# Kernel tuning notes

Measured on AMD Instinct MI355X. Metric: run time of the kernel, lower is better.

## Reference

```python
import jax, jax.numpy as jnp
import numpy as np

B, T, D_IN, D, OUT, L, NDAYS = 32, 2048, 512, 256, 41, 3, 45
INNER = 2 * D  # expand=2

def silu(x):
    return x * jax.nn.sigmoid(x)

def layernorm(x, s, b, eps=1e-5):
    m = x.mean(-1, keepdims=True)
    v = ((x - m) ** 2).mean(-1, keepdims=True)
    return (x - m) / jnp.sqrt(v + eps) * s + b

def dwconv(x, k, b):
    # x: [B,T,C], k: [C,4] depthwise kernel, b: [C]
    # torch Conv1d(padding=2)[..., :T] == pad (left=2, right=1), valid window 4
    y = jax.lax.conv_general_dilated(
        x.transpose(0, 2, 1), k[:, None, :], window_strides=(1,),
        padding=[(2, 1)], feature_group_count=k.shape[0],
        dimension_numbers=('NCH', 'OIH', 'NCH'))
    return y.transpose(0, 2, 1) + b

def soft_window(x, Win, convK, convB, dtW, dtB, Wout):
    # x: [B,T,D]
    xz = x @ Win                      # [B,T,2*INNER]
    xi, z = jnp.split(xz, 2, axis=-1)
    xc = silu(dwconv(xi, convK, convB))
    dt = jax.nn.softplus(xc @ dtW + dtB)
    w = jnp.exp(-jnp.cumsum(dt, axis=1) * 0.1)
    return (xc * w * silu(z)) @ Wout  # [B,T,D]

def setup_inputs() -> dict:
    key = jax.random.key(0)
    ks = iter(jax.random.split(key, 40))
    n = lambda shp, s=0.02: jax.random.normal(next(ks), shp, dtype=jnp.float32) * s
    inp = {}
    inp['x'] = jax.random.normal(next(ks), (B, T, D_IN), dtype=jnp.float32)
    inp['day_ids'] = jax.random.randint(next(ks), (B,), 0, NDAYS)
    inp['adapter_W'] = jnp.tile(jnp.eye(D_IN)[None], (NDAYS, 1, 1)) + n((NDAYS, D_IN, D_IN))
    inp['adapter_b'] = n((NDAYS, D_IN))
    inp['cW1'] = n((D_IN, D)); inp['cb1'] = n((D,))
    inp['cln1_s'] = jnp.ones((D,)); inp['cln1_b'] = jnp.zeros((D,))
    inp['cW2'] = n((D, D)); inp['cb2'] = n((D,))
    inp['cln2_s'] = jnp.ones((D,)); inp['cln2_b'] = jnp.zeros((D,))
    # mamba params: leading dims [L, 2] for (fwd, bwd) directions
    inp['m_in'] = n((L, 2, D, 2 * INNER))
    inp['m_convK'] = n((L, 2, INNER, 4), 0.2); inp['m_convB'] = n((L, 2, INNER))
    inp['m_dtW'] = n((L, 2, INNER, INNER)); inp['m_dtB'] = n((L, 2, INNER))
    inp['m_out'] = n((L, 2, INNER, D))
    inp['proj_W'] = n((L, 2 * D, D)); inp['proj_b'] = n((L, D))
    inp['norm_s'] = jnp.ones((L, D)); inp['norm_b'] = jnp.zeros((L, D))
    inp['outW'] = n((D, OUT)); inp['outb'] = n((OUT,))
    return inp

def reference(x, day_ids, adapter_W, adapter_b, cW1, cb1, cln1_s, cln1_b,
              cW2, cb2, cln2_s, cln2_b, m_in, m_convK, m_convB, m_dtW, m_dtB,
              m_out, proj_W, proj_b, norm_s, norm_b, outW, outb):
    # Day adapter: batched gather-matmul (replaces per-sample python loop)
    h = jnp.einsum('btd,bde->bte', x, adapter_W[day_ids]) + adapter_b[day_ids][:, None, :]
    h = jax.nn.soft_sign(h)
    # input compress MLP (dropout = eval identity)
    h = silu(layernorm(h @ cW1 + cb1, cln1_s, cln1_b))
    h = silu(layernorm(h @ cW2 + cb2, cln2_s, cln2_b))
    # stacked bidirectional pseudo-SSM layers
    for l in range(L):
        fwd = soft_window(h, m_in[l, 0], m_convK[l, 0], m_convB[l, 0],
                          m_dtW[l, 0], m_dtB[l, 0], m_out[l, 0])
        hr = h[:, ::-1, :]
        bwd = soft_window(hr, m_in[l, 1], m_convK[l, 1], m_convB[l, 1],
                          m_dtW[l, 1], m_dtB[l, 1], m_out[l, 1])[:, ::-1, :]
        combined = jnp.concatenate([fwd, bwd], axis=-1) @ proj_W[l] + proj_b[l]
        h = layernorm(h + combined, norm_s[l], norm_b[l])
    return jax.nn.log_softmax(h @ outW + outb, axis=-1)
```

## Files before the change

### kernel.cpp

```cpp
#include <hip/hip_runtime.h>
#include <hip/hip_bf16.h>
#include <cstdint>
#include <math.h>

typedef __bf16 bf16_t;
typedef bf16_t bf16x8 __attribute__((ext_vector_type(8)));
typedef bf16_t bf16x4 __attribute__((ext_vector_type(4)));
typedef float f32x4 __attribute__((ext_vector_type(4)));

#define B_ 32
#define T_ 2048
#define D_ 256
#define INNER_ 512
#define L_ 3
#define CHUNK_ 64
#define NCHUNK_ (T_/CHUNK_)

typedef const __attribute__((address_space(1))) void* gas_t;
typedef __attribute__((address_space(3))) void* las_t;
__device__ __forceinline__ void gll16(const void* g, void* l) {
  __builtin_amdgcn_global_load_lds((gas_t)g, (las_t)l, 16, 0, 0);
}

struct GemmP {
  const bf16_t* A;
  const bf16_t* Bt;
  const float* bias;
  float* outF;
  bf16_t* outB;
  float* sums;
  const int* day_ids;
  long bStrideBt;
  int bStrideBias;
  int K, N, ldout, colOff, act, revA, revC, nValid;
};

__device__ __forceinline__ int csw(int row, int colByte) {
  return (row << 8) + (colByte ^ ((row & 7) << 4));
}

__global__ __launch_bounds__(256, 4)
void gemm_kernel(GemmP p) {
  __shared__ char smem[32768];
  bf16_t* As = (bf16_t*)smem;
  bf16_t* Bs = (bf16_t*)(smem + 16384);
  const int tid = threadIdx.x;
  const int wave = tid >> 6, lane = tid & 63;

  const int nb = p.N >> 7;
  const int nbs = __builtin_ctz(nb);
  const int c8 = blockIdx.x & 7;
  const int k8 = blockIdx.x >> 3;
  const int mGrp = (gridDim.x >> 3) >> nbs;
  const int m0 = (c8 * mGrp + (k8 >> nbs)) << 7;
  const int n0 = (k8 & (nb - 1)) << 7;

  const bf16_t* Bt = p.Bt;
  const float* bias = p.bias;
  if (p.day_ids) {
    int day = p.day_ids[m0 >> 11];
    Bt += (long)day * p.bStrideBt;
    if (bias) bias += (long)day * p.bStrideBias;
  }
  const int K = p.K;
  const int srow = tid >> 2;
  const int sc = ((tid & 3) - (tid >> 4)) & 3;
  const int sk = sc << 3;

  int ar0 = m0 + srow, ar1 = m0 + srow + 64;
  if (p.revA) {
    int t0 = ar0 & (T_-1); ar0 = ar0 - t0 + (T_-1 - t0);
    int t1 = ar1 & (T_-1); ar1 = ar1 - t1 + (T_-1 - t1);
  }
  const bf16_t* aP0 = p.A + (long)ar0 * K + sk;
  const bf16_t* aP1 = p.A + (long)ar1 * K + sk;
  const bf16_t* bP0 = Bt + (long)(n0 + srow) * K + sk;
  const bf16_t* bP1 = bP0 + (long)64 * K;

  char* aL = (char*)As + wave * 1024;
  char* bL = (char*)Bs + wave * 1024;

  f32x4 acc[4][4] = {};
  const int mw = ((wave >> 1) << 6), nw = ((wave & 1) << 6);
  const int fr = lane & 15;
  const int foff = (((lane >> 4) + (fr >> 2)) & 3) << 4;

  gll16(aP0, aL);
  gll16(aP1, aL + 4096);
  gll16(bP0, bL);
  gll16(bP1, bL + 4096);
  __syncthreads();

  const int nIter = K >> 5;
  for (int it = 0; it < nIter; ++it) {
    const int cur = (it & 1) << 13;
    const int nxt = cur ^ 8192;
    if (it + 1 < nIter) {
      const int k1 = (it + 1) << 5;
      gll16(aP0 + k1, aL + nxt);
      gll16(aP1 + k1, aL + nxt + 4096);
      gll16(bP0 + k1, bL + nxt);
      gll16(bP1 + k1, bL + nxt + 4096);
    }
    bf16x8 af[4], bfr[4];
#pragma unroll
    for (int i = 0; i < 4; i++)
      af[i] = *(const bf16x8*)((char*)As + cur + (mw + i*16 + fr)*64 + foff);
#pragma unroll
    for (int j = 0; j < 4; j++)
      bfr[j] = *(const bf16x8*)((char*)Bs + cur + (nw + j*16 + fr)*64 + foff);
#pragma unroll
    for (int im = 0; im < 4; im++)
#pragma unroll
      for (int in = 0; in < 4; in++)
        acc[im][in] = __builtin_amdgcn_mfma_f32_16x16x32_bf16(bfr[in], af[im], acc[im][in], 0, 0, 0);
    __syncthreads();
  }

  const int cn = lane & 15, rq = (lane >> 4) << 2;
  f32x4 csum[4];
#pragma unroll
  for (int in = 0; in < 4; in++) csum[in] = (f32x4){0.f,0.f,0.f,0.f};

#pragma unroll
  for (int im = 0; im < 4; im++) {
    int trow = mw + im*16 + cn;
#pragma unroll
    for (int in = 0; in < 4; in++) {
      int tcolB = (nw + in*16 + rq) << 1;
      int colb = n0 + nw + in*16 + rq;
      f32x4 v = acc[im][in];
      if (bias) {
        f32x4 bv = *(const f32x4*)(bias + colb);
        v = v + bv;
      }
      if (p.act == 1) {
#pragma unroll
        for (int r = 0; r < 4; r++) v[r] = v[r] / (1.f + fabsf(v[r]));
      } else if (p.act >= 2) {
#pragma unroll
        for (int r = 0; r < 4; r++) {
          float e = __expf(-fabsf(v[r]));
          v[r] = fmaxf(v[r], 0.f) + __logf(1.f + e);
        }
      }
      if (p.act == 3) csum[in] = csum[in] + v;
      if (p.outB) {
        bf16x4 o;
#pragma unroll
        for (int r = 0; r < 4; r++) o[r] = (bf16_t)v[r];
        *(bf16x4*)(smem + csw(trow, tcolB)) = o;
      }
      if (p.outF) {
        int gr = m0 + trow;
        int orow = gr;
        if (p.revC) { int t = gr & (T_-1); orow = gr - t + (T_-1 - t); }
        long rowOff = (long)orow * p.ldout + p.colOff;
#pragma unroll
        for (int r = 0; r < 4; r++) {
          int col = colb + r;
          if (col < p.nValid) p.outF[rowOff + col] = v[r];
        }
      }
    }
  }

  if (p.act == 3) {
#pragma unroll
    for (int in = 0; in < 4; in++) {
#pragma unroll
      for (int b = 1; b < 16; b <<= 1) {
#pragma unroll
        for (int r = 0; r < 4; r++) csum[in][r] += __shfl_xor(csum[in][r], b);
      }
    }
    if (cn == 0) {
      int chunk = (m0 + mw) >> 6;
#pragma unroll
      for (int in = 0; in < 4; in++)
        *(f32x4*)(p.sums + (long)chunk * INNER_ + n0 + nw + in*16 + rq) = csum[in];
    }
  }

  if (p.outB) {
    __syncthreads();
    const int rsub = tid >> 4;
    const int cb16 = (tid & 15) << 4;
#pragma unroll
    for (int itr = 0; itr < 8; ++itr) {
      int trow = (itr << 4) + rsub;
      bf16x8 val = *(const bf16x8*)(smem + csw(trow, cb16));
      int gr = m0 + trow;
      int orow = gr;
      if (p.revC) { int t = gr & (T_-1); orow = gr - t + (T_-1 - t); }
      long off = (long)orow * p.ldout + p.colOff + n0 + (cb16 >> 1);
      *(bf16x8*)(p.outB + off) = val;
    }
  }
}

__global__ __launch_bounds__(256)
void ln_kernel(const bf16_t* in, const bf16_t* resid, const float* s, const float* bb,
               bf16_t* outB, int doSilu) {
  int row = (blockIdx.x << 2) + (threadIdx.x >> 6);
  int lane = threadIdx.x & 63;
  long base = (long)row * D_ + (lane << 2);
  bf16x4 iv = *(const bf16x4*)(in + base);
  float v[4];
#pragma unroll
  for (int k = 0; k < 4; k++) v[k] = (float)iv[k];
  if (resid) {
    bf16x4 rv = *(const bf16x4*)(resid + base);
#pragma unroll
    for (int k = 0; k < 4; k++) v[k] += (float)rv[k];
  }
  float s1 = v[0] + v[1] + v[2] + v[3];
  float s2 = v[0]*v[0] + v[1]*v[1] + v[2]*v[2] + v[3]*v[3];
#pragma unroll
  for (int off = 1; off < 64; off <<= 1) {
    s1 += __shfl_xor(s1, off);
    s2 += __shfl_xor(s2, off);
  }
  float mean = s1 * (1.f / D_);
  float var = s2 * (1.f / D_) - mean * mean;
  float inv = rsqrtf(var + 1e-5f);
  f32x4 sv = *(const f32x4*)(s + (lane << 2));
  f32x4 bv = *(const f32x4*)(bb + (lane << 2));
  bf16x4 ov;
#pragma unroll
  for (int k = 0; k < 4; k++) {
    float val = (v[k] - mean) * inv * sv[k] + bv[k];
    if (doSilu) val = val / (1.f + __expf(-val));
    ov[k] = (bf16_t)val;
  }
  *(bf16x4*)(outB + base) = ov;
}

__global__ __launch_bounds__(256)
void conv_kernel(const bf16_t* xz, const float* K4, const float* cb, bf16_t* xc) {
  long idx = (long)blockIdx.x * 256 + threadIdx.x;
  int ch0 = ((int)(idx & 63)) << 3;
  long bt = idx >> 6;
  int t = (int)(bt & (T_-1));
  const bf16_t* base = xz + bt * (2*INNER_) + ch0;
  bf16x8 r0, r1, r2, r3;
  r2 = *(const bf16x8*)(base);
#pragma unroll
  for (int k = 0; k < 8; k++) { r0[k] = (bf16_t)0.f; r1[k] = (bf16_t)0.f; r3[k] = (bf16_t)0.f; }
  if (t >= 2) r0 = *(const bf16x8*)(base - 2*(2*INNER_));
  if (t >= 1) r1 = *(const bf16x8*)(base - (2*INNER_));
  if (t < T_-1) r3 = *(const bf16x8*)(base + (2*INNER_));
  bf16x8 o8;
#pragma unroll
  for (int k = 0; k < 8; k++) {
    f32x4 kk = *(const f32x4*)(K4 + ((ch0 + k) << 2));
    float a = cb[ch0 + k] + (float)r0[k]*kk[0] + (float)r1[k]*kk[1]
            + (float)r2[k]*kk[2] + (float)r3[k]*kk[3];
    o8[k] = (bf16_t)(a / (1.f + __expf(-a)));
  }
  *(bf16x8*)(xc + bt * INNER_ + ch0) = o8;
}

__global__ __launch_bounds__(256)
void y_kernel(const bf16_t* dt, const bf16_t* xz, bf16_t* xc, const float* sums) {
  int bc = blockIdx.x * 4 + (threadIdx.x >> 6);
  int b = bc >> 5;
  int c = bc & 31;
  int ch0 = (threadIdx.x & 63) << 3;
  float acc[8] = {};
  const float* sp = sums + (long)b * NCHUNK_ * INNER_ + ch0;
  for (int cp = 0; cp < c; cp++) {
#pragma unroll
    for (int k = 0; k < 8; k++) acc[k] += sp[(long)cp * INNER_ + k];
  }
  long bt0 = (long)bc * CHUNK_;
  for (int i = 0; i < CHUNK_; i++) {
    long bt = bt0 + i;
    bf16x8 d8 = *(const bf16x8*)(dt + bt * INNER_ + ch0);
    bf16x8 z8 = *(const bf16x8*)(xz + bt * (2*INNER_) + INNER_ + ch0);
    bf16x8 x8 = *(const bf16x8*)(xc + bt * INNER_ + ch0);
    bf16x8 o8;
#pragma unroll
    for (int k = 0; k < 8; k++) {
      acc[k] += (float)d8[k];
      float w = __expf(-0.1f * acc[k]);
      float zz = (float)z8[k];
      float sz = zz / (1.f + __expf(-zz));
      o8[k] = (bf16_t)((float)x8[k] * w * sz);
    }
    *(bf16x8*)(xc + bt * INNER_ + ch0) = o8;
  }
}

__global__ __launch_bounds__(256)
void lsm_kernel(const float* logits, float* out) {
  int row = (blockIdx.x << 2) + (threadIdx.x >> 6);
  int lane = threadIdx.x & 63;
  float v = (lane < 41) ? logits[(long)row * 41 + lane] : -3.4e38f;
  float m = v;
#pragma unroll
  for (int off = 1; off < 64; off <<= 1) m = fmaxf(m, __shfl_xor(m, off));
  float e = (lane < 41) ? __expf(v - m) : 0.f;
  float ssum = e;
#pragma unroll
  for (int off = 1; off < 64; off <<= 1) ssum += __shfl_xor(ssum, off);
  float ls = __logf(ssum);
  if (lane < 41) out[(long)row * 41 + lane] = v - m - ls;
}

__global__ void tconv_kernel(const float* in, bf16_t* out, int R, int C) {
  __shared__ float tile[32][33];
  const float* ip = in + (long)blockIdx.z * R * C;
  bf16_t* op = out + (long)blockIdx.z * R * C;
  int c0 = blockIdx.x << 5, r0 = blockIdx.y << 5;
  int tx = threadIdx.x, ty = threadIdx.y;
  for (int i = ty; i < 32; i += 8) {
    int r = r0 + i, c = c0 + tx;
    tile[i][tx] = (r < R && c < C) ? ip[(long)r * C + c] : 0.f;
  }
  __syncthreads();
  for (int i = ty; i < 32; i += 8) {
    int c = c0 + i, r = r0 + tx;
    if (c < C && r < R) op[(long)c * R + r] = (bf16_t)tile[tx][i];
  }
}

__global__ void cvt_kernel(const float* in, bf16_t* out, long n) {
  long i = ((long)blockIdx.x * blockDim.x + threadIdx.x) << 3;
  if (i >= n) return;
  f32x4 a = *(const f32x4*)(in + i);
  f32x4 b = *(const f32x4*)(in + i + 4);
  bf16x8 o;
#pragma unroll
  for (int k = 0; k < 4; k++) { o[k] = (bf16_t)a[k]; o[k+4] = (bf16_t)b[k]; }
  *(bf16x8*)(out + i) = o;
}

__global__ void zfill_kernel(bf16_t* p, int n) {
  int i = blockIdx.x * 256 + threadIdx.x;
  if (i < n) p[i] = (bf16_t)0.f;
}

extern "C" void kernel_launch(void* const* d_in, const int* in_sizes, int n_in,
                              void* d_out, int out_size, void* d_ws, size_t ws_size,
                              hipStream_t stream) {
  (void)in_sizes; (void)n_in; (void)out_size;
  const float* x         = (const float*)d_in[0];
  const int*   day_ids   = (const int*)d_in[1];
  const float* adapter_W = (const float*)d_in[2];
  const float* adapter_b = (const float*)d_in[3];
  const float* cW1       = (const float*)d_in[4];
  const float* cb1       = (const float*)d_in[5];
  const float* cln1_s    = (const float*)d_in[6];
  const float* cln1_b    = (const float*)d_in[7];
  const float* cW2       = (const float*)d_in[8];
  const float* cb2       = (const float*)d_in[9];
  const float* cln2_s    = (const float*)d_in[10];
  const float* cln2_b    = (const float*)d_in[11];
  const float* m_in      = (const float*)d_in[12];
  const float* m_convK   = (const float*)d_in[13];
  const float* m_convB   = (const float*)d_in[14];
  const float* m_dtW     = (const float*)d_in[15];
  const float* m_dtB     = (const float*)d_in[16];
  const float* m_out     = (const float*)d_in[17];
  const float* proj_W    = (const float*)d_in[18];
  const float* proj_b    = (const float*)d_in[19];
  const float* norm_s    = (const float*)d_in[20];
  const float* norm_b    = (const float*)d_in[21];
  const float* outW      = (const float*)d_in[22];
  const float* outb      = (const float*)d_in[23];
  float* out = (float*)d_out;

  char* ws = (char*)d_ws;
  size_t off = 0;
  auto alloc = [&](size_t bytes) -> char* {
    char* p = ws + off;
    off += (bytes + 255) & ~(size_t)255;
    return p;
  };
  bf16_t* adapterT = (bf16_t*)alloc((size_t)45*512*512*2);
  bf16_t* cW1T     = (bf16_t*)alloc((size_t)256*512*2);
  bf16_t* cW2T     = (bf16_t*)alloc((size_t)256*256*2);
  bf16_t* m_inT    = (bf16_t*)alloc((size_t)6*1024*256*2);
  bf16_t* m_dtWT   = (bf16_t*)alloc((size_t)6*512*512*2);
  bf16_t* m_outT   = (bf16_t*)alloc((size_t)6*256*512*2);
  bf16_t* projT    = (bf16_t*)alloc((size_t)3*256*512*2);
  bf16_t* outWT    = (bf16_t*)alloc((size_t)128*256*2);

  int Bg = 0;
  {
    const int cands[6] = {32, 16, 8, 4, 2, 1};
    for (int ci = 0; ci < 6; ci++) {
      int c = cands[ci];
      size_t Mg = (size_t)c * T_;
      size_t need = Mg*2048 + 3*(Mg*1024) + Mg*512 + (size_t)c*NCHUNK_*INNER_*4
                    + 8*256;
      if (off + need <= ws_size) { Bg = c; break; }
    }
  }
  if (Bg == 0) return;
  const size_t Mg = (size_t)Bg * T_;
  char*  xzR  = alloc(Mg * 2048);
  char*  xcR  = alloc(Mg * 1024);
  char*  dtR  = alloc(Mg * 1024);
  char*  swR  = alloc(Mg * 1024);
  bf16_t* hG  = (bf16_t*)alloc(Mg * 512);
  float* sums = (float*)alloc((size_t)Bg * NCHUNK_ * INNER_ * 4);

  zfill_kernel<<<128, 256, 0, stream>>>(outWT, 128*256);
  dim3 tb(32, 8);
  tconv_kernel<<<dim3(16,16,45), tb, 0, stream>>>(adapter_W, adapterT, 512, 512);
  tconv_kernel<<<dim3(8,16,1),  tb, 0, stream>>>(cW1,  cW1T,  512, 256);
  tconv_kernel<<<dim3(8,8,1),   tb, 0, stream>>>(cW2,  cW2T,  256, 256);
  tconv_kernel<<<dim3(32,8,6),  tb, 0, stream>>>(m_in, m_inT, 256, 1024);
  tconv_kernel<<<dim3(16,16,6), tb, 0, stream>>>(m_dtW, m_dtWT, 512, 512);
  tconv_kernel<<<dim3(8,16,6),  tb, 0, stream>>>(m_out, m_outT, 512, 256);
  tconv_kernel<<<dim3(8,16,3),  tb, 0, stream>>>(proj_W, projT, 512, 256);
  tconv_kernel<<<dim3(2,8,1),   tb, 0, stream>>>(outW, outWT, 256, 41);

  auto gemm = [&](const bf16_t* A, const bf16_t* Bt, const float* bias,
                  float* outF, bf16_t* outB, int K, int N, int ldout, int colOff,
                  int act, int revA, int revC, const int* days, long bsBt, int bsBias,
                  int nValid, float* sumsP) {
    GemmP p;
    p.A = A; p.Bt = Bt; p.bias = bias; p.outF = outF; p.outB = outB; p.sums = sumsP;
    p.day_ids = days; p.bStrideBt = bsBt; p.bStrideBias = bsBias;
    p.K = K; p.N = N; p.ldout = ldout; p.colOff = colOff;
    p.act = act; p.revA = revA; p.revC = revC; p.nValid = nValid;
    gemm_kernel<<<dim3((unsigned)((Mg/128) * (N/128))), 256, 0, stream>>>(p);
  };

  for (int b0 = 0; b0 < B_; b0 += Bg) {
    const float* xg = x + (size_t)b0 * T_ * 512;

    bf16_t* x_bf = (bf16_t*)xzR;
    cvt_kernel<<<(unsigned)(Mg/4), 256, 0, stream>>>(xg, x_bf, (long)Mg*512);

    bf16_t* h0 = (bf16_t*)xcR;
    gemm(x_bf, adapterT, adapter_b, nullptr, h0, 512, 512, 512, 0, 1, 0, 0,
         day_ids + b0, (long)512*512, 512, 512, nullptr);

    bf16_t* tmpB = (bf16_t*)dtR;
    gemm(h0, cW1T, cb1, nullptr, tmpB, 512, 256, 256, 0, 0, 0, 0, nullptr, 0, 0, 256, nullptr);
    bf16_t* h1 = (bf16_t*)swR;
    ln_kernel<<<(unsigned)(Mg/4), 256, 0, stream>>>(tmpB, nullptr, cln1_s, cln1_b, h1, 1);

    gemm(h1, cW2T, cb2, nullptr, tmpB, 256, 256, 256, 0, 0, 0, 0, nullptr, 0, 0, 256, nullptr);
    ln_kernel<<<(unsigned)(Mg/4), 256, 0, stream>>>(tmpB, nullptr, cln2_s, cln2_b, hG, 1);

    bf16_t* xz    = (bf16_t*)xzR;
    bf16_t* xc    = (bf16_t*)xcR;
    bf16_t* dt    = (bf16_t*)dtR;
    bf16_t* swcat = (bf16_t*)swR;

    for (int l = 0; l < L_; l++) {
      for (int dir = 0; dir < 2; dir++) {
        int ld = l*2 + dir;
        gemm(hG, m_inT + (size_t)ld*1024*256, nullptr, nullptr, xz,
             256, 1024, 1024, 0, 0, dir, 0, nullptr, 0, 0, 1024, nullptr);
        conv_kernel<<<(unsigned)(Mg/4), 256, 0, stream>>>(
            xz, m_convK + (size_t)ld*512*4, m_convB + (size_t)ld*512, xc);
        gemm(xc, m_dtWT + (size_t)ld*512*512, m_dtB + (size_t)ld*512, nullptr, dt,
             512, 512, 512, 0, 3, 0, 0, nullptr, 0, 0, 512, sums);
        y_kernel<<<(unsigned)(Bg*8), 256, 0, stream>>>(dt, xz, xc, sums);
        gemm(xc, m_outT + (size_t)ld*256*512, nullptr, nullptr, swcat,
             512, 256, 512, dir*256, 0, 0, dir, nullptr, 0, 0, 256, nullptr);
      }
      bf16_t* tmpB2 = (bf16_t*)dtR;
      gemm(swcat, projT + (size_t)l*256*512, proj_b + (size_t)l*256, nullptr, tmpB2,
           512, 256, 256, 0, 0, 0, 0, nullptr, 0, 0, 256, nullptr);
      ln_kernel<<<(unsigned)(Mg/4), 256, 0, stream>>>(tmpB2, hG, norm_s + (size_t)l*256,
                                                      norm_b + (size_t)l*256, hG, 0);
    }

    float* logits = (float*)xzR;
    gemm(hG, outWT, outb, logits, nullptr, 256, 128, 41, 0, 0, 0, 0,
         nullptr, 0, 0, 41, nullptr);
    lsm_kernel<<<(unsigned)(Mg/4), 256, 0, stream>>>(logits, out + (size_t)b0 * T_ * 41);
  }
}
```

Before: 2.413 ms.

## Shrink cumsum chunks to 16 rows and add separate prefix-scan kernel

The GEMM epilogue now writes per-16-row partial sums of dt instead of per-64-row sums, and a new scan kernel turns these into exclusive prefix offsets per batch and channel. The y kernel then reads a single precomputed offset and walks only 16 timesteps per thread group, using four times as many blocks. This removes the quadratic prefix re-summation in y_kernel and raises parallelism, at the cost of an extra serial scan launch over 128 chunks per channel and more shuffle reductions in the epilogue.

```diff
diff --git a/kernel.cpp b/kernel.cpp
--- a/kernel.cpp
+++ b/kernel.cpp
@@ -13,8 +13,8 @@
 #define D_ 256
 #define INNER_ 512
 #define L_ 3
-#define CHUNK_ 64
-#define NCHUNK_ (T_/CHUNK_)
+#define CH16_ 16
+#define NCH16_ (T_/CH16_)
 
 typedef const __attribute__((address_space(1))) void* gas_t;
 typedef __attribute__((address_space(3))) void* las_t;
@@ -118,13 +118,11 @@
   }
 
   const int cn = lane & 15, rq = (lane >> 4) << 2;
-  f32x4 csum[4];
-#pragma unroll
-  for (int in = 0; in < 4; in++) csum[in] = (f32x4){0.f,0.f,0.f,0.f};
 
 #pragma unroll
   for (int im = 0; im < 4; im++) {
     int trow = mw + im*16 + cn;
+    f32x4 cs[4];
 #pragma unroll
     for (int in = 0; in < 4; in++) {
       int tcolB = (nw + in*16 + rq) << 1;
@@ -144,7 +142,7 @@
           v[r] = fmaxf(v[r], 0.f) + __logf(1.f + e);
         }
       }
-      if (p.act == 3) csum[in] = csum[in] + v;
+      cs[in] = v;
       if (p.outB) {
         bf16x4 o;
 #pragma unroll
@@ -163,22 +161,21 @@
         }
       }
     }
-  }
-
-  if (p.act == 3) {
-#pragma unroll
-    for (int in = 0; in < 4; in++) {
-#pragma unroll
-      for (int b = 1; b < 16; b <<= 1) {
-#pragma unroll
-        for (int r = 0; r < 4; r++) csum[in][r] += __shfl_xor(csum[in][r], b);
-      }
-    }
-    if (cn == 0) {
-      int chunk = (m0 + mw) >> 6;
-#pragma unroll
-      for (int in = 0; in < 4; in++)
-        *(f32x4*)(p.sums + (long)chunk * INNER_ + n0 + nw + in*16 + rq) = csum[in];
+    if (p.act == 3) {
+#pragma unroll
+      for (int in = 0; in < 4; in++) {
+#pragma unroll
+        for (int b = 1; b < 16; b <<= 1) {
+#pragma unroll
+          for (int r = 0; r < 4; r++) cs[in][r] += __shfl_xor(cs[in][r], b);
+        }
+      }
+      if (cn == 0) {
+        int chunk16 = ((m0 + mw) >> 4) + im;
+#pragma unroll
+        for (int in = 0; in < 4; in++)
+          *(f32x4*)(p.sums + (long)chunk16 * INNER_ + n0 + nw + in*16 + rq) = cs[in];
+      }
     }
   }
 
@@ -262,19 +259,31 @@
 }
 
 __global__ __launch_bounds__(256)
+void scan_kernel(float* sums) {
+  int id = blockIdx.x * 256 + threadIdx.x;
+  int b = id >> 9, ch = id & 511;
+  float* sp = sums + (long)b * NCH16_ * INNER_ + ch;
+  float run = 0.f;
+#pragma unroll 4
+  for (int c = 0; c < NCH16_; c++) {
+    float v = sp[(long)c << 9];
+    sp[(long)c << 9] = run;
+    run += v;
+  }
+}
+
+__global__ __launch_bounds__(256)
 void y_kernel(const bf16_t* dt, const bf16_t* xz, bf16_t* xc, const float* sums) {
   int bc = blockIdx.x * 4 + (threadIdx.x >> 6);
-  int b = bc >> 5;
-  int c = bc & 31;
   int ch0 = (threadIdx.x & 63) << 3;
-  float acc[8] = {};
-  const float* sp = sums + (long)b * NCHUNK_ * INNER_ + ch0;
-  for (int cp = 0; cp < c; cp++) {
-#pragma unroll
-    for (int k = 0; k < 8; k++) acc[k] += sp[(long)cp * INNER_ + k];
-  }
-  long bt0 = (long)bc * CHUNK_;
-  for (int i = 0; i < CHUNK_; i++) {
+  const float* sp = sums + (long)bc * INNER_ + ch0;
+  float acc[8];
+  f32x4 a0 = *(const f32x4*)sp, a1 = *(const f32x4*)(sp + 4);
+#pragma unroll
+  for (int k = 0; k < 4; k++) { acc[k] = a0[k]; acc[k+4] = a1[k]; }
+  long bt0 = (long)bc * CH16_;
+#pragma unroll
+  for (int i = 0; i < CH16_; i++) {
     long bt = bt0 + i;
     bf16x8 d8 = *(const bf16x8*)(dt + bt * INNER_ + ch0);
     bf16x8 z8 = *(const bf16x8*)(xz + bt * (2*INNER_) + INNER_ + ch0);
@@ -393,7 +402,7 @@
     for (int ci = 0; ci < 6; ci++) {
       int c = cands[ci];
       size_t Mg = (size_t)c * T_;
-      size_t need = Mg*2048 + 3*(Mg*1024) + Mg*512 + (size_t)c*NCHUNK_*INNER_*4
+      size_t need = Mg*2048 + 3*(Mg*1024) + Mg*512 + (size_t)c*NCH16_*INNER_*4
                     + 8*256;
       if (off + need <= ws_size) { Bg = c; break; }
     }
@@ -405,7 +414,7 @@
   char*  dtR  = alloc(Mg * 1024);
   char*  swR  = alloc(Mg * 1024);
   bf16_t* hG  = (bf16_t*)alloc(Mg * 512);
-  float* sums = (float*)alloc((size_t)Bg * NCHUNK_ * INNER_ * 4);
+  float* sums = (float*)alloc((size_t)Bg * NCH16_ * INNER_ * 4);
 
   zfill_kernel<<<128, 256, 0, stream>>>(outWT, 128*256);
   dim3 tb(32, 8);
@@ -462,7 +471,8 @@
             xz, m_convK + (size_t)ld*512*4, m_convB + (size_t)ld*512, xc);
         gemm(xc, m_dtWT + (size_t)ld*512*512, m_dtB + (size_t)ld*512, nullptr, dt,
              512, 512, 512, 0, 3, 0, 0, nullptr, 0, 0, 512, sums);
-        y_kernel<<<(unsigned)(Bg*8), 256, 0, stream>>>(dt, xz, xc, sums);
+        scan_kernel<<<(unsigned)(Bg*2), 256, 0, stream>>>(sums);
+        y_kernel<<<(unsigned)(Mg/64), 256, 0, stream>>>(dt, xz, xc, sums);
         gemm(xc, m_outT + (size_t)ld*256*512, nullptr, nullptr, swcat,
              512, 256, 512, dir*256, 0, 0, dir, nullptr, 0, 0, 256, nullptr);
       }
```

Result: no change. 2.421 ms (+0.3%).
